# Kernel optimization log

Hardware: AMD Instinct MI355X
Metric: run time of the kernel (lower is better)

The kernel has to match this reference:

```python
import jax, jax.numpy as jnp
import numpy as np

N = 100000       # nodes
E = 1600000      # edges (before self loops)
G = 64           # graphs in batch
IN, HID, OUT = 128, 64, 16
NEG_SLOPE = 0.2  # PyG GATConv default


def setup_inputs() -> dict:
    key = jax.random.key(0)
    ks = jax.random.split(key, 16)
    s = 0.1  # weight init scale
    return {
        "x": jax.random.normal(ks[0], (N, IN), dtype=jnp.float32),
        "edge_index": jax.random.randint(ks[1], (2, E), 0, N, dtype=jnp.int32),
        "batch": jnp.sort(jax.random.randint(ks[2], (N,), 0, G, dtype=jnp.int32)),
        "W1": jax.random.normal(ks[3], (IN, 2 * HID), dtype=jnp.float32) * s,
        "a_src1": jax.random.normal(ks[4], (2, HID), dtype=jnp.float32) * s,
        "a_dst1": jax.random.normal(ks[5], (2, HID), dtype=jnp.float32) * s,
        "b1": jax.random.normal(ks[6], (2 * HID,), dtype=jnp.float32) * s,
        "W2": jax.random.normal(ks[7], (2 * HID, HID), dtype=jnp.float32) * s,
        "a_src2": jax.random.normal(ks[8], (1, HID), dtype=jnp.float32) * s,
        "a_dst2": jax.random.normal(ks[9], (1, HID), dtype=jnp.float32) * s,
        "b2": jax.random.normal(ks[10], (HID,), dtype=jnp.float32) * s,
        "dw1": jax.random.normal(ks[11], (HID, HID), dtype=jnp.float32) * s,
        "db1": jax.random.normal(ks[12], (HID,), dtype=jnp.float32) * s,
        "dw2": jax.random.normal(ks[13], (HID, OUT), dtype=jnp.float32) * s,
        "db2": jax.random.normal(ks[14], (OUT,), dtype=jnp.float32) * s,
    }


def gat_conv(x, src, dst, W, a_src, a_dst, b):
    """PyG GATConv (concat=True, self-loops already appended to src/dst)."""
    n = x.shape[0]
    heads, out = a_src.shape
    h = (x @ W).reshape(n, heads, out)                       # [N,H,O]
    e_src = jnp.einsum("nho,ho->nh", h, a_src)               # [N,H]
    e_dst = jnp.einsum("nho,ho->nh", h, a_dst)
    e = jax.nn.leaky_relu(e_src[src] + e_dst[dst], NEG_SLOPE)  # [E',H]
    # segment softmax over incoming edges of each destination node
    m = jax.lax.stop_gradient(jax.ops.segment_max(e, dst, num_segments=n))
    a = jnp.exp(e - m[dst])
    denom = jax.ops.segment_sum(a, dst, num_segments=n)
    alpha = a / denom[dst]                                   # [E',H]
    msg = h[src] * alpha[:, :, None]                         # [E',H,O]
    agg = jax.ops.segment_sum(msg, dst, num_segments=n)      # [N,H,O]
    return agg.reshape(n, heads * out) + b


def reference(x, edge_index, batch, W1, a_src1, a_dst1, b1, W2, a_src2, a_dst2,
              b2, dw1, db1, dw2, db2):
    n = x.shape[0]
    loops = jnp.arange(n, dtype=edge_index.dtype)            # add_self_loops=True
    src = jnp.concatenate([edge_index[0], loops])
    dst = jnp.concatenate([edge_index[1], loops])

    h = jax.nn.relu(gat_conv(x, src, dst, W1, a_src1, a_dst1, b1))   # [N,128]
    h = gat_conv(h, src, dst, W2, a_src2, a_dst2, b2)                # [N,64]

    # global mean pool over graphs
    cnt = jax.ops.segment_sum(jnp.ones((n,), h.dtype), batch, num_segments=G)
    pooled = jax.ops.segment_sum(h, batch, num_segments=G)
    pooled = pooled / jnp.maximum(cnt, 1.0)[:, None]                  # [G,64]

    # decoder MLP (dropout inactive in eval)
    z = jax.nn.relu(pooled @ dw1 + db1)
    return z @ dw2 + db2                                              # [G,16]
```

## Files before the change

### kernel.cpp

```cpp
#include <hip/hip_runtime.h>
#include <stdint.h>


#define LRELU(x) ((x) > 0.f ? (x) : 0.2f * (x))
#define LOG2E 1.4426950408889634f
#define BCAP 3072
#define PSLICE 8

typedef short bf8 __attribute__((ext_vector_type(8)));
typedef float f32x4 __attribute__((ext_vector_type(4)));
typedef float f32x2 __attribute__((ext_vector_type(2)));

__device__ __forceinline__ uint16_t f2bf(float f) {
  uint32_t u = __float_as_uint(f);
  u += 0x7fff + ((u >> 16) & 1);
  return (uint16_t)(u >> 16);
}
__device__ __forceinline__ uint32_t pack2bf(float a, float b) {
  return (uint32_t)f2bf(a) | ((uint32_t)f2bf(b) << 16);
}
__device__ __forceinline__ uint8_t f2fp8(float v) {
  return (uint8_t)(__builtin_amdgcn_cvt_pk_fp8_f32(v, v, 0, false) & 0xff);
}
__device__ __forceinline__ void fp8x4_to_f32(uint32_t v, float* o) {
  f32x2 lo = __builtin_amdgcn_cvt_pk_f32_fp8(v, false);
  f32x2 hi = __builtin_amdgcn_cvt_pk_f32_fp8(v, true);
  o[0] = lo[0]; o[1] = lo[1]; o[2] = hi[0]; o[3] = hi[1];
}


__global__ __launch_bounds__(256) void scatter_cvt_kernel(
    const int* __restrict__ ei, int* __restrict__ bcur,
    uint32_t* __restrict__ bpack, const float* __restrict__ W1,
    const float* __restrict__ W2, uint16_t* __restrict__ WT1,
    uint16_t* __restrict__ WT2, int E, int E2, int shift, int nb, int gCH) {
  int blk = blockIdx.x;
  int t = threadIdx.x;
  if (blk >= gCH) {
    int idx = (blk - gCH) * 256 + t;
    if (idx < 128 * 128) {
      int n = idx >> 7, k = idx & 127;
      WT1[idx] = f2bf(W1[(size_t)k * 128 + n]);
    } else if (idx < 128 * 128 + 64 * 128) {
      int j = idx - 128 * 128;
      int n = j >> 7, k = j & 127;
      WT2[j] = f2bf(W2[(size_t)k * 64 + n]);
    }
    return;
  }
  __shared__ int lh[1024];
  __shared__ int lb[1024];
  for (int i = t; i < 1024; i += 256) lh[i] = 0;
  __syncthreads();
  int base = blk * 4096;
  int bszm1 = (1 << shift) - 1;
  uint32_t pk[16];
  int rk[16], bk[16];
#pragma unroll
  for (int u = 0; u < 16; ++u) {
    int e = base + u * 256 + t;
    if (e < E2) {
      int s, d;
      if (e < E) { s = ei[e]; d = ei[E + e]; } else { s = d = e - E; }
      bk[u] = d >> shift;
      pk[u] = ((uint32_t)s << shift) | (uint32_t)(d & bszm1);
      rk[u] = atomicAdd(&lh[bk[u]], 1);
    } else rk[u] = -1;
  }
  __syncthreads();
  for (int i = t; i < nb; i += 256) {
    int c = lh[i];
    lb[i] = c ? atomicAdd(&bcur[i], c) : 0;
  }
  __syncthreads();
#pragma unroll
  for (int u = 0; u < 16; ++u) {
    if (rk[u] >= 0) {
      int pos = lb[bk[u]] + rk[u];
      if (pos < BCAP) bpack[(size_t)bk[u] * BCAP + pos] = pk[u];
    }
  }
}


__device__ __forceinline__ void bfinal_body(const uint32_t* __restrict__ bpack,
                                            const int* __restrict__ bcur,
                                            int2* __restrict__ off2,
                                            int* __restrict__ ssrc, int N,
                                            int shift, int b) {
  __shared__ int hist[512];
  __shared__ int loff[512];
  __shared__ int ssc[256];
  __shared__ int lsrc[BCAP];
  int t = threadIdx.x;
  int bsz = 1 << shift;
  int node0 = b << shift;
  int e0 = b * BCAP;
  int cnt = min(bcur[b], BCAP);
  for (int i = t; i < bsz; i += 256) hist[i] = 0;
  __syncthreads();
  uint32_t pe[12];
  int ne = 0;
#pragma unroll
  for (int j = 0; j < 12; ++j) {
    int i = j * 256 + t;
    if (i < cnt) { pe[j] = bpack[(size_t)b * BCAP + i]; ne = j + 1; }
  }
  int bszm1 = bsz - 1;
  for (int j = 0; j < ne; ++j) atomicAdd(&hist[pe[j] & bszm1], 1);
  __syncthreads();
  int per = (bsz + 255) >> 8;
  int basei = t * per;
  int va[2] = {0, 0};
  int sum = 0;
#pragma unroll 2
  for (int j = 0; j < per; ++j) {
    if (basei + j < bsz) va[j] = hist[basei + j];
    sum += va[j];
  }
  ssc[t] = sum;
  __syncthreads();
  for (int d = 1; d < 256; d <<= 1) {
    int x = (t >= d) ? ssc[t - d] : 0;
    __syncthreads();
    ssc[t] += x;
    __syncthreads();
  }
  int run = ssc[t] - sum;
#pragma unroll 2
  for (int j = 0; j < per; ++j) {
    if (basei + j < bsz) {
      loff[basei + j] = run;
      int v = node0 + basei + j;
      if (v < N) off2[v] = make_int2(e0 + run, e0 + run + va[j]);
      run += va[j];
    }
  }
  for (int i = t; i < bsz; i += 256) hist[i] = 0;
  __syncthreads();
  for (int j = 0; j < ne; ++j) {
    int ld = pe[j] & bszm1;
    int r = atomicAdd(&hist[ld], 1);
    lsrc[loff[ld] + r] = (int)(pe[j] >> shift);
  }
  __syncthreads();
  for (int i = t; i < cnt; i += 256) ssrc[e0 + i] = lsrc[i];
}


template <int N, int HEADS, int AFP32>
__device__ __forceinline__ void gemm_body(const void* __restrict__ Av,
                                          const uint16_t* __restrict__ WT,
                                          uint8_t* __restrict__ C,
                                          const float* __restrict__ aS,
                                          const float* __restrict__ aD,
                                          float* __restrict__ es,
                                          float* __restrict__ ed, int M, int blk) {
  constexpr int CT = N / 16;
  int wave = threadIdx.x >> 6;
  int lane = threadIdx.x & 63;
  int m16 = lane & 15;
  int quad = lane >> 4;
  int row_base = blk * 128 + wave * 32;
  if (row_base >= M) return;
  const uint16_t* Ab0 = (const uint16_t*)Av + (size_t)(row_base + m16) * 128;
  const uint16_t* Ab1 = Ab0 + (size_t)16 * 128;
  const float* Af0 = (const float*)Av + (size_t)(row_base + m16) * 128;
  const float* Af1 = Af0 + (size_t)16 * 128;
  f32x4 acc[2][CT] = {};
#pragma unroll
  for (int ks = 0; ks < 4; ++ks) {
    int k0 = ks * 32 + quad * 8;
    bf8 a0, a1;
    if (AFP32) {
      float4 v0 = *reinterpret_cast<const float4*>(Af0 + k0);
      float4 v1 = *reinterpret_cast<const float4*>(Af0 + k0 + 4);
      uint4 pk0;
      pk0.x = pack2bf(v0.x, v0.y); pk0.y = pack2bf(v0.z, v0.w);
      pk0.z = pack2bf(v1.x, v1.y); pk0.w = pack2bf(v1.z, v1.w);
      a0 = *reinterpret_cast<bf8*>(&pk0);
      float4 w0 = *reinterpret_cast<const float4*>(Af1 + k0);
      float4 w1 = *reinterpret_cast<const float4*>(Af1 + k0 + 4);
      uint4 pk1;
      pk1.x = pack2bf(w0.x, w0.y); pk1.y = pack2bf(w0.z, w0.w);
      pk1.z = pack2bf(w1.x, w1.y); pk1.w = pack2bf(w1.z, w1.w);
      a1 = *reinterpret_cast<bf8*>(&pk1);
    } else {
      a0 = *reinterpret_cast<const bf8*>(Ab0 + k0);
      a1 = *reinterpret_cast<const bf8*>(Ab1 + k0);
    }
#pragma unroll
    for (int c = 0; c < CT; ++c) {
      bf8 b = *reinterpret_cast<const bf8*>(WT + (size_t)(c * 16 + m16) * 128 + k0);
      acc[0][c] = __builtin_amdgcn_mfma_f32_16x16x32_bf16(a0, b, acc[0][c], 0, 0, 0);
      acc[1][c] = __builtin_amdgcn_mfma_f32_16x16x32_bf16(a1, b, acc[1][c], 0, 0, 0);
    }
  }
#pragma unroll
  for (int r = 0; r < 2; ++r) {
#pragma unroll
    for (int c = 0; c < CT; ++c) {
#pragma unroll
      for (int reg = 0; reg < 4; ++reg) {
        int row = row_base + r * 16 + quad * 4 + reg;
        C[(size_t)row * N + c * 16 + m16] = f2fp8(acc[r][c][reg]);
      }
    }
  }
  float aSv[CT], aDv[CT];
#pragma unroll
  for (int c = 0; c < CT; ++c) {
    aSv[c] = aS[c * 16 + m16];
    aDv[c] = aD[c * 16 + m16];
  }
#pragma unroll
  for (int r = 0; r < 2; ++r) {
#pragma unroll
    for (int reg = 0; reg < 4; ++reg) {
      float es0 = 0.f, es1 = 0.f, ed0 = 0.f, ed1 = 0.f;
#pragma unroll
      for (int c = 0; c < CT; ++c) {
        float v = acc[r][c][reg];
        if (HEADS == 2 && c >= CT / 2) {
          es1 = fmaf(v, aSv[c], es1);
          ed1 = fmaf(v, aDv[c], ed1);
        } else {
          es0 = fmaf(v, aSv[c], es0);
          ed0 = fmaf(v, aDv[c], ed0);
        }
      }
#pragma unroll
      for (int o = 1; o < 16; o <<= 1) {
        es0 += __shfl_xor(es0, o);
        ed0 += __shfl_xor(ed0, o);
        if (HEADS == 2) {
          es1 += __shfl_xor(es1, o);
          ed1 += __shfl_xor(ed1, o);
        }
      }
      if (m16 == 0) {
        int row = row_base + r * 16 + quad * 4 + reg;
        if (HEADS == 2) {
          es[row * 2] = es0 * LOG2E; es[row * 2 + 1] = es1 * LOG2E;
          ed[row * 2] = ed0 * LOG2E; ed[row * 2 + 1] = ed1 * LOG2E;
        } else {
          es[row] = es0 * LOG2E;
          ed[row] = ed0 * LOG2E;
        }
      }
    }
  }
}


__global__ __launch_bounds__(256) void gemm1_bfinal_kernel(
    const float* __restrict__ x, const uint16_t* __restrict__ WT1,
    uint8_t* __restrict__ hb1, const float* __restrict__ aS,
    const float* __restrict__ aD, float* __restrict__ es, float* __restrict__ ed,
    int M, const uint32_t* __restrict__ bpack, const int* __restrict__ bcur,
    int2* __restrict__ off2, int* __restrict__ ssrc, int shift, int gM) {
  int blk = blockIdx.x;
  if (blk < gM) {
    gemm_body<128, 2, 1>(x, WT1, hb1, aS, aD, es, ed, M, blk);
  } else {
    bfinal_body(bpack, bcur, off2, ssrc, M, shift, blk - gM);
  }
}

template <int N, int HEADS, int AFP32>
__global__ __launch_bounds__(256) void gemm_mfma(const void* __restrict__ Av,
                                                 const uint16_t* __restrict__ WT,
                                                 uint8_t* __restrict__ C,
                                                 const float* __restrict__ aS,
                                                 const float* __restrict__ aD,
                                                 float* __restrict__ es,
                                                 float* __restrict__ ed, int M) {
  gemm_body<N, HEADS, AFP32>(Av, WT, C, aS, aD, es, ed, M, blockIdx.x);
}


__global__ void agg1_kernel(const uint4* __restrict__ h16, const float* __restrict__ es,
                            const float2* __restrict__ ed, const int2* __restrict__ off2,
                            const int* __restrict__ ssrc, const float* __restrict__ b,
                            uint4* __restrict__ outb4, int n) {
  int w = __builtin_amdgcn_readfirstlane((blockIdx.x * 256 + threadIdx.x) >> 6);
  int lane = threadIdx.x & 63;
  if (w >= n) return;
  int sub = lane >> 3;
  int q = lane & 7;
  bool hi = q >= 4;
  float2 edw = ed[w];
  float edh = hi ? edw.y : edw.x;
  const float* esp = es + (hi ? 1 : 0);
  float acc[16] = {};
  float den = 0.f;
  int2 oo = off2[w];
  int e0 = oo.x, e1 = oo.y;
  int base = e0;
  for (; base + 16 <= e1; base += 16) {
    int s0 = ssrc[base + sub];
    int s1 = ssrc[base + 8 + sub];
    float ev0 = esp[2 * s0];
    float ev1 = esp[2 * s1];
    uint4 g0 = h16[(size_t)s0 * 8 + q];
    uint4 g1 = h16[(size_t)s1 * 8 + q];
    float a0 = exp2f(LRELU(ev0 + edh));
    float a1 = exp2f(LRELU(ev1 + edh));
    den += a0 + a1;
    float f0[16], f1[16];
    fp8x4_to_f32(g0.x, f0); fp8x4_to_f32(g0.y, f0 + 4);
    fp8x4_to_f32(g0.z, f0 + 8); fp8x4_to_f32(g0.w, f0 + 12);
    fp8x4_to_f32(g1.x, f1); fp8x4_to_f32(g1.y, f1 + 4);
    fp8x4_to_f32(g1.z, f1 + 8); fp8x4_to_f32(g1.w, f1 + 12);
#pragma unroll
    for (int j = 0; j < 16; ++j) acc[j] = fmaf(a0, f0[j], acc[j]);
#pragma unroll
    for (int j = 0; j < 16; ++j) acc[j] = fmaf(a1, f1[j], acc[j]);
  }
  if (base + 8 <= e1) {
    int s0 = ssrc[base + sub];
    float ev0 = esp[2 * s0];
    uint4 g0 = h16[(size_t)s0 * 8 + q];
    float a0 = exp2f(LRELU(ev0 + edh));
    den += a0;
    float f0[16];
    fp8x4_to_f32(g0.x, f0); fp8x4_to_f32(g0.y, f0 + 4);
    fp8x4_to_f32(g0.z, f0 + 8); fp8x4_to_f32(g0.w, f0 + 12);
#pragma unroll
    for (int j = 0; j < 16; ++j) acc[j] = fmaf(a0, f0[j], acc[j]);
    base += 8;
  }
  int e = base + sub;
  if (e < e1) {
    int s0 = ssrc[e];
    float ev0 = esp[2 * s0];
    uint4 g0 = h16[(size_t)s0 * 8 + q];
    float a0 = exp2f(LRELU(ev0 + edh));
    den += a0;
    float f0[16];
    fp8x4_to_f32(g0.x, f0); fp8x4_to_f32(g0.y, f0 + 4);
    fp8x4_to_f32(g0.z, f0 + 8); fp8x4_to_f32(g0.w, f0 + 12);
#pragma unroll
    for (int j = 0; j < 16; ++j) acc[j] = fmaf(a0, f0[j], acc[j]);
  }
#pragma unroll
  for (int m = 8; m <= 32; m <<= 1) {
    den += __shfl_xor(den, m);
#pragma unroll
    for (int j = 0; j < 16; ++j) acc[j] += __shfl_xor(acc[j], m);
  }
  if (sub == 0) {
    float inv = 1.0f / den;
    float o[16];
#pragma unroll
    for (int k = 0; k < 4; ++k) {
      float4 bb = reinterpret_cast<const float4*>(b)[q * 4 + k];
      o[k * 4 + 0] = fmaxf(fmaf(acc[k * 4 + 0], inv, bb.x), 0.f);
      o[k * 4 + 1] = fmaxf(fmaf(acc[k * 4 + 1], inv, bb.y), 0.f);
      o[k * 4 + 2] = fmaxf(fmaf(acc[k * 4 + 2], inv, bb.z), 0.f);
      o[k * 4 + 3] = fmaxf(fmaf(acc[k * 4 + 3], inv, bb.w), 0.f);
    }
    uint4 oA, oB;
    oA.x = pack2bf(o[0], o[1]);   oA.y = pack2bf(o[2], o[3]);
    oA.z = pack2bf(o[4], o[5]);   oA.w = pack2bf(o[6], o[7]);
    oB.x = pack2bf(o[8], o[9]);   oB.y = pack2bf(o[10], o[11]);
    oB.z = pack2bf(o[12], o[13]); oB.w = pack2bf(o[14], o[15]);
    outb4[(size_t)w * 16 + q * 2] = oA;
    outb4[(size_t)w * 16 + q * 2 + 1] = oB;
  }
}


__global__ void agg2_pool_kernel(const uint2* __restrict__ h8,
                                 const float* __restrict__ es,
                                 const float* __restrict__ ed,
                                 const int2* __restrict__ off2,
                                 const int* __restrict__ ssrc,
                                 const float* __restrict__ b,
                                 const int* __restrict__ batch,
                                 float* __restrict__ pooled, int gstride, int n) {
  int w = __builtin_amdgcn_readfirstlane((blockIdx.x * 256 + threadIdx.x) >> 6);
  int wave = threadIdx.x >> 6;
  int lane = threadIdx.x & 63;
  bool act = (w < n);
  int sub = lane >> 3;
  int q = lane & 7;
  __shared__ float red[4][64];
  __shared__ int gidS[4];
  float acc[8] = {};
  float den = 1.f;
  if (act) {
    float edw = ed[w];
    den = 0.f;
    int2 oo = off2[w];
    int e0 = oo.x, e1 = oo.y;
    int base = e0;
    for (; base + 16 <= e1; base += 16) {
      int s0 = ssrc[base + sub];
      int s1 = ssrc[base + 8 + sub];
      float ev0 = es[s0];
      float ev1 = es[s1];
      uint2 g0 = h8[(size_t)s0 * 8 + q];
      uint2 g1 = h8[(size_t)s1 * 8 + q];
      float a0 = exp2f(LRELU(ev0 + edw));
      float a1 = exp2f(LRELU(ev1 + edw));
      den += a0 + a1;
      float f0[8], f1[8];
      fp8x4_to_f32(g0.x, f0); fp8x4_to_f32(g0.y, f0 + 4);
      fp8x4_to_f32(g1.x, f1); fp8x4_to_f32(g1.y, f1 + 4);
#pragma unroll
      for (int j = 0; j < 8; ++j) acc[j] = fmaf(a0, f0[j], acc[j]);
#pragma unroll
      for (int j = 0; j < 8; ++j) acc[j] = fmaf(a1, f1[j], acc[j]);
    }
    if (base + 8 <= e1) {
      int s0 = ssrc[base + sub];
      float ev0 = es[s0];
      uint2 g0 = h8[(size_t)s0 * 8 + q];
      float a0 = exp2f(LRELU(ev0 + edw));
      den += a0;
      float f0[8];
      fp8x4_to_f32(g0.x, f0); fp8x4_to_f32(g0.y, f0 + 4);
#pragma unroll
      for (int j = 0; j < 8; ++j) acc[j] = fmaf(a0, f0[j], acc[j]);
      base += 8;
    }
    int e = base + sub;
    if (e < e1) {
      int s0 = ssrc[e];
      float ev0 = es[s0];
      uint2 g0 = h8[(size_t)s0 * 8 + q];
      float a0 = exp2f(LRELU(ev0 + edw));
      den += a0;
      float f0[8];
      fp8x4_to_f32(g0.x, f0); fp8x4_to_f32(g0.y, f0 + 4);
#pragma unroll
      for (int j = 0; j < 8; ++j) acc[j] = fmaf(a0, f0[j], acc[j]);
    }
#pragma unroll
    for (int m = 8; m <= 32; m <<= 1) {
      den += __shfl_xor(den, m);
#pragma unroll
      for (int j = 0; j < 8; ++j) acc[j] += __shfl_xor(acc[j], m);
    }
    if (sub == 0) {
      float inv = 1.0f / den;
      float4 b0 = reinterpret_cast<const float4*>(b)[q * 2];
      float4 b1 = reinterpret_cast<const float4*>(b)[q * 2 + 1];
      red[wave][q * 8 + 0] = fmaf(acc[0], inv, b0.x);
      red[wave][q * 8 + 1] = fmaf(acc[1], inv, b0.y);
      red[wave][q * 8 + 2] = fmaf(acc[2], inv, b0.z);
      red[wave][q * 8 + 3] = fmaf(acc[3], inv, b0.w);
      red[wave][q * 8 + 4] = fmaf(acc[4], inv, b1.x);
      red[wave][q * 8 + 5] = fmaf(acc[5], inv, b1.y);
      red[wave][q * 8 + 6] = fmaf(acc[6], inv, b1.z);
      red[wave][q * 8 + 7] = fmaf(acc[7], inv, b1.w);
    }
  }
  if (lane == 0) gidS[wave] = act ? batch[w] : -1;
  __syncthreads();
  float* pslice = pooled + (size_t)(blockIdx.x & (PSLICE - 1)) * gstride;
  int g0 = gidS[0];
  bool uni = (g0 >= 0) & (gidS[1] == g0) & (gidS[2] == g0) & (gidS[3] == g0);
  int t = threadIdx.x;
  if (uni) {
    if (t < 64) {
      float s = red[0][t] + red[1][t] + red[2][t] + red[3][t];
      atomicAdd(&pslice[g0 * 64 + t], s);
    }
  } else {
    int wv = t >> 6, c = t & 63;
    int g = gidS[wv];
    if (g >= 0) atomicAdd(&pslice[g * 64 + c], red[wv][c]);
  }
}


__device__ __forceinline__ int lowerb(const int* __restrict__ a, int n, int v) {
  int lo = 0, hi = n;
  while (lo < hi) {
    int mid = (lo + hi) >> 1;
    if (a[mid] < v) lo = mid + 1; else hi = mid;
  }
  return lo;
}

__global__ void mlp_kernel(const float* __restrict__ pooled, int gstride,
                           const int* __restrict__ batch, int n,
                           const float* __restrict__ dw1, const float* __restrict__ db1,
                           const float* __restrict__ dw2, const float* __restrict__ db2,
                           float* __restrict__ out) {
  int g = blockIdx.x;
  int c = threadIdx.x;
  __shared__ float P[64];
  __shared__ float Z[64];
  __shared__ int cntS;
  if (c == 0) cntS = lowerb(batch, n, g + 1) - lowerb(batch, n, g);
  __syncthreads();
  float inv = 1.0f / fmaxf((float)cntS, 1.0f);
  float p = 0.f;
#pragma unroll
  for (int s = 0; s < PSLICE; ++s) p += pooled[(size_t)s * gstride + g * 64 + c];
  P[c] = p * inv;
  __syncthreads();
  float s = db1[c];
#pragma unroll
  for (int k = 0; k < 64; ++k) s = fmaf(P[k], dw1[k * 64 + c], s);
  Z[c] = fmaxf(s, 0.f);
  __syncthreads();
  if (c < 16) {
    float s2 = db2[c];
#pragma unroll
    for (int k = 0; k < 64; ++k) s2 = fmaf(Z[k], dw2[k * 16 + c], s2);
    out[g * 16 + c] = s2;
  }
}


extern "C" void kernel_launch(void* const* d_in, const int* in_sizes, int n_in,
                              void* d_out, int out_size, void* d_ws, size_t ws_size,
                              hipStream_t stream) {
  const float* x      = (const float*)d_in[0];
  const int*   ei     = (const int*)d_in[1];
  const int*   batch  = (const int*)d_in[2];
  const float* W1     = (const float*)d_in[3];
  const float* a_src1 = (const float*)d_in[4];
  const float* a_dst1 = (const float*)d_in[5];
  const float* b1     = (const float*)d_in[6];
  const float* W2     = (const float*)d_in[7];
  const float* a_src2 = (const float*)d_in[8];
  const float* a_dst2 = (const float*)d_in[9];
  const float* b2     = (const float*)d_in[10];
  const float* dw1    = (const float*)d_in[11];
  const float* db1    = (const float*)d_in[12];
  const float* dw2    = (const float*)d_in[13];
  const float* db2    = (const float*)d_in[14];
  float* out = (float*)d_out;

  const int N = in_sizes[2];
  const int E = in_sizes[1] / 2;
  const int E2 = E + N;
  const int G = out_size / 16;
  const int gstride = G * 64;

  int shift = 7;
  while ((N >> shift) >= 1024) ++shift;
  const int NB = ((N - 1) >> shift) + 1;

  char* ws = (char*)d_ws;
  size_t o = 0;
  auto alloc = [&](size_t bytes) {
    void* p = ws + o;
    o = (o + bytes + 255) & ~(size_t)255;
    return p;
  };
  int*      zreg   = (int*)alloc((size_t)(1024 + PSLICE * gstride) * 4);
  int*      bcur   = zreg;
  float*    pooled = (float*)(zreg + 1024);
  int2*     off2   = (int2*)alloc((size_t)N * 8);
  uint32_t* bpack  = (uint32_t*)alloc((size_t)NB * BCAP * 4);
  int*      ssrc   = (int*)alloc((size_t)NB * BCAP * 4);
  float*    es1    = (float*)alloc((size_t)N * 2 * 4);
  float*    ed1    = (float*)alloc((size_t)N * 2 * 4);
  float*    es2    = (float*)alloc((size_t)N * 4);
  float*    ed2    = (float*)alloc((size_t)N * 4);
  uint16_t* wt1b   = (uint16_t*)alloc((size_t)128 * 128 * 2);
  uint16_t* wt2b   = (uint16_t*)alloc((size_t)64 * 128 * 2);
  uint8_t*  hb1    = (uint8_t*)alloc((size_t)N * 128);
  uint8_t*  hb2    = (uint8_t*)alloc((size_t)N * 64);
  uint32_t* out1b  = (uint32_t*)alloc((size_t)N * 64 * 4);

  hipMemsetAsync(zreg, 0, (size_t)(1024 + PSLICE * gstride) * 4, stream);

  int gM   = (N + 127) / 128;
  int gW   = (N + 3) / 4;
  int gCH  = (E2 + 4095) / 4096;
  int gCVT = (128 * 128 + 64 * 128 + 255) / 256;

  scatter_cvt_kernel<<<gCH + gCVT, 256, 0, stream>>>(ei, bcur, bpack, W1, W2,
                                                     wt1b, wt2b, E, E2, shift,
                                                     NB, gCH);
  gemm1_bfinal_kernel<<<gM + NB, 256, 0, stream>>>(x, wt1b, hb1, a_src1, a_dst1,
                                                   es1, ed1, N, bpack, bcur,
                                                   off2, ssrc, shift, gM);
  agg1_kernel<<<gW, 256, 0, stream>>>((const uint4*)hb1, es1,
                                      (const float2*)ed1, off2, ssrc, b1,
                                      (uint4*)out1b, N);
  gemm_mfma<64, 1, 0><<<gM, 256, 0, stream>>>((const void*)out1b, wt2b, hb2,
                                              a_src2, a_dst2, es2, ed2, N);
  agg2_pool_kernel<<<gW, 256, 0, stream>>>((const uint2*)hb2, es2, ed2, off2,
                                           ssrc, b2, batch, pooled, gstride, N);
  mlp_kernel<<<G, 64, 0, stream>>>(pooled, gstride, batch, N, dw1, db1, dw2,
                                   db2, out);
}
```

Before: 309.7 us.

## Map one node per 8-lane group in GAT aggregation kernels instead of per wave

Both aggregation kernels now give each node to an 8-lane subgroup, so one wave handles 8 destination nodes. Each subgroup walks the node's edges serially, unrolled by 4, which removes the cross-subgroup shuffle reduction and lane underuse on low-degree nodes. The grid shrinks by 8x to match. In the pooling kernel, wave-uniform graph ids are reduced by shuffles and then through shared memory. Mixed-graph waves fall back to per-lane atomics. The cost is a serial dependency chain per node and divergence across lanes when node degrees differ.

```diff
diff --git a/kernel.cpp b/kernel.cpp
--- a/kernel.cpp
+++ b/kernel.cpp
@@ -26,6 +26,19 @@
   f32x2 lo = __builtin_amdgcn_cvt_pk_f32_fp8(v, false);
   f32x2 hi = __builtin_amdgcn_cvt_pk_f32_fp8(v, true);
   o[0] = lo[0]; o[1] = lo[1]; o[2] = hi[0]; o[3] = hi[1];
+}
+__device__ __forceinline__ void a1_edge(const uint4& gv, float av, float* acc) {
+  float f[16];
+  fp8x4_to_f32(gv.x, f);     fp8x4_to_f32(gv.y, f + 4);
+  fp8x4_to_f32(gv.z, f + 8); fp8x4_to_f32(gv.w, f + 12);
+#pragma unroll
+  for (int j = 0; j < 16; ++j) acc[j] = fmaf(av, f[j], acc[j]);
+}
+__device__ __forceinline__ void a2_edge(const uint2& gv, float av, float* acc) {
+  float f[8];
+  fp8x4_to_f32(gv.x, f); fp8x4_to_f32(gv.y, f + 4);
+#pragma unroll
+  for (int j = 0; j < 8; ++j) acc[j] = fmaf(av, f[j], acc[j]);
 }
 
 
@@ -283,91 +296,63 @@
                             const float2* __restrict__ ed, const int2* __restrict__ off2,
                             const int* __restrict__ ssrc, const float* __restrict__ b,
                             uint4* __restrict__ outb4, int n) {
-  int w = __builtin_amdgcn_readfirstlane((blockIdx.x * 256 + threadIdx.x) >> 6);
+  int wv = __builtin_amdgcn_readfirstlane((blockIdx.x * 256 + threadIdx.x) >> 6);
   int lane = threadIdx.x & 63;
+  int grp = lane >> 3;
+  int cl = lane & 7;
+  int w = wv * 8 + grp;
   if (w >= n) return;
-  int sub = lane >> 3;
-  int q = lane & 7;
-  bool hi = q >= 4;
+  bool hi = cl >= 4;
   float2 edw = ed[w];
   float edh = hi ? edw.y : edw.x;
   const float* esp = es + (hi ? 1 : 0);
   float acc[16] = {};
   float den = 0.f;
   int2 oo = off2[w];
-  int e0 = oo.x, e1 = oo.y;
-  int base = e0;
-  for (; base + 16 <= e1; base += 16) {
-    int s0 = ssrc[base + sub];
-    int s1 = ssrc[base + 8 + sub];
-    float ev0 = esp[2 * s0];
-    float ev1 = esp[2 * s1];
-    uint4 g0 = h16[(size_t)s0 * 8 + q];
-    uint4 g1 = h16[(size_t)s1 * 8 + q];
-    float a0 = exp2f(LRELU(ev0 + edh));
-    float a1 = exp2f(LRELU(ev1 + edh));
-    den += a0 + a1;
-    float f0[16], f1[16];
-    fp8x4_to_f32(g0.x, f0); fp8x4_to_f32(g0.y, f0 + 4);
-    fp8x4_to_f32(g0.z, f0 + 8); fp8x4_to_f32(g0.w, f0 + 12);
-    fp8x4_to_f32(g1.x, f1); fp8x4_to_f32(g1.y, f1 + 4);
-    fp8x4_to_f32(g1.z, f1 + 8); fp8x4_to_f32(g1.w, f1 + 12);
-#pragma unroll
-    for (int j = 0; j < 16; ++j) acc[j] = fmaf(a0, f0[j], acc[j]);
-#pragma unroll
-    for (int j = 0; j < 16; ++j) acc[j] = fmaf(a1, f1[j], acc[j]);
-  }
-  if (base + 8 <= e1) {
-    int s0 = ssrc[base + sub];
-    float ev0 = esp[2 * s0];
-    uint4 g0 = h16[(size_t)s0 * 8 + q];
-    float a0 = exp2f(LRELU(ev0 + edh));
+  int e = oo.x, e1 = oo.y;
+  for (; e + 4 <= e1; e += 4) {
+    int s0 = ssrc[e];
+    int s1 = ssrc[e + 1];
+    int s2 = ssrc[e + 2];
+    int s3 = ssrc[e + 3];
+    uint4 g0 = h16[(size_t)s0 * 8 + cl];
+    uint4 g1 = h16[(size_t)s1 * 8 + cl];
+    uint4 g2 = h16[(size_t)s2 * 8 + cl];
+    uint4 g3 = h16[(size_t)s3 * 8 + cl];
+    float a0 = exp2f(LRELU(esp[2 * s0] + edh));
+    float a1 = exp2f(LRELU(esp[2 * s1] + edh));
+    float a2 = exp2f(LRELU(esp[2 * s2] + edh));
+    float a3 = exp2f(LRELU(esp[2 * s3] + edh));
+    den += (a0 + a1) + (a2 + a3);
+    a1_edge(g0, a0, acc);
+    a1_edge(g1, a1, acc);
+    a1_edge(g2, a2, acc);
+    a1_edge(g3, a3, acc);
+  }
+  for (; e < e1; ++e) {
+    int s0 = ssrc[e];
+    uint4 g0 = h16[(size_t)s0 * 8 + cl];
+    float a0 = exp2f(LRELU(esp[2 * s0] + edh));
     den += a0;
-    float f0[16];
-    fp8x4_to_f32(g0.x, f0); fp8x4_to_f32(g0.y, f0 + 4);
-    fp8x4_to_f32(g0.z, f0 + 8); fp8x4_to_f32(g0.w, f0 + 12);
-#pragma unroll
-    for (int j = 0; j < 16; ++j) acc[j] = fmaf(a0, f0[j], acc[j]);
-    base += 8;
-  }
-  int e = base + sub;
-  if (e < e1) {
-    int s0 = ssrc[e];
-    float ev0 = esp[2 * s0];
-    uint4 g0 = h16[(size_t)s0 * 8 + q];
-    float a0 = exp2f(LRELU(ev0 + edh));
-    den += a0;
-    float f0[16];
-    fp8x4_to_f32(g0.x, f0); fp8x4_to_f32(g0.y, f0 + 4);
-    fp8x4_to_f32(g0.z, f0 + 8); fp8x4_to_f32(g0.w, f0 + 12);
-#pragma unroll
-    for (int j = 0; j < 16; ++j) acc[j] = fmaf(a0, f0[j], acc[j]);
-  }
-#pragma unroll
-  for (int m = 8; m <= 32; m <<= 1) {
-    den += __shfl_xor(den, m);
-#pragma unroll
-    for (int j = 0; j < 16; ++j) acc[j] += __shfl_xor(acc[j], m);
-  }
-  if (sub == 0) {
-    float inv = 1.0f / den;
-    float o[16];
-#pragma unroll
-    for (int k = 0; k < 4; ++k) {
-      float4 bb = reinterpret_cast<const float4*>(b)[q * 4 + k];
-      o[k * 4 + 0] = fmaxf(fmaf(acc[k * 4 + 0], inv, bb.x), 0.f);
-      o[k * 4 + 1] = fmaxf(fmaf(acc[k * 4 + 1], inv, bb.y), 0.f);
-      o[k * 4 + 2] = fmaxf(fmaf(acc[k * 4 + 2], inv, bb.z), 0.f);
-      o[k * 4 + 3] = fmaxf(fmaf(acc[k * 4 + 3], inv, bb.w), 0.f);
-    }
-    uint4 oA, oB;
-    oA.x = pack2bf(o[0], o[1]);   oA.y = pack2bf(o[2], o[3]);
-    oA.z = pack2bf(o[4], o[5]);   oA.w = pack2bf(o[6], o[7]);
-    oB.x = pack2bf(o[8], o[9]);   oB.y = pack2bf(o[10], o[11]);
-    oB.z = pack2bf(o[12], o[13]); oB.w = pack2bf(o[14], o[15]);
-    outb4[(size_t)w * 16 + q * 2] = oA;
-    outb4[(size_t)w * 16 + q * 2 + 1] = oB;
-  }
+    a1_edge(g0, a0, acc);
+  }
+  float inv = 1.0f / den;
+  float o[16];
+#pragma unroll
+  for (int k = 0; k < 4; ++k) {
+    float4 bb = reinterpret_cast<const float4*>(b)[cl * 4 + k];
+    o[k * 4 + 0] = fmaxf(fmaf(acc[k * 4 + 0], inv, bb.x), 0.f);
+    o[k * 4 + 1] = fmaxf(fmaf(acc[k * 4 + 1], inv, bb.y), 0.f);
+    o[k * 4 + 2] = fmaxf(fmaf(acc[k * 4 + 2], inv, bb.z), 0.f);
+    o[k * 4 + 3] = fmaxf(fmaf(acc[k * 4 + 3], inv, bb.w), 0.f);
+  }
+  uint4 oA, oB;
+  oA.x = pack2bf(o[0], o[1]);   oA.y = pack2bf(o[2], o[3]);
+  oA.z = pack2bf(o[4], o[5]);   oA.w = pack2bf(o[6], o[7]);
+  oB.x = pack2bf(o[8], o[9]);   oB.y = pack2bf(o[10], o[11]);
+  oB.z = pack2bf(o[12], o[13]); oB.w = pack2bf(o[14], o[15]);
+  outb4[(size_t)w * 16 + cl * 2] = oA;
+  outb4[(size_t)w * 16 + cl * 2 + 1] = oB;
 }
 
 
@@ -379,99 +364,95 @@
                                  const float* __restrict__ b,
                                  const int* __restrict__ batch,
                                  float* __restrict__ pooled, int gstride, int n) {
-  int w = __builtin_amdgcn_readfirstlane((blockIdx.x * 256 + threadIdx.x) >> 6);
-  int wave = threadIdx.x >> 6;
-  int lane = threadIdx.x & 63;
+  int t = threadIdx.x;
+  int wv = __builtin_amdgcn_readfirstlane((blockIdx.x * 256 + t) >> 6);
+  int wave = t >> 6;
+  int lane = t & 63;
+  int grp = lane >> 3;
+  int cl = lane & 7;
+  int w = wv * 8 + grp;
   bool act = (w < n);
-  int sub = lane >> 3;
-  int q = lane & 7;
   __shared__ float red[4][64];
-  __shared__ int gidS[4];
+  __shared__ int uniS[4];
+  float* pslice = pooled + (size_t)(blockIdx.x & (PSLICE - 1)) * gstride;
   float acc[8] = {};
-  float den = 1.f;
+  int g = -1;
   if (act) {
+    g = batch[w];
     float edw = ed[w];
-    den = 0.f;
+    float den = 0.f;
     int2 oo = off2[w];
-    int e0 = oo.x, e1 = oo.y;
-    int base = e0;
-    for (; base + 16 <= e1; base += 16) {
-      int s0 = ssrc[base + sub];
-      int s1 = ssrc[base + 8 + sub];
-      float ev0 = es[s0];
-      float ev1 = es[s1];
-      uint2 g0 = h8[(size_t)s0 * 8 + q];
-      uint2 g1 = h8[(size_t)s1 * 8 + q];
-      float a0 = exp2f(LRELU(ev0 + edw));
-      float a1 = exp2f(LRELU(ev1 + edw));
-      den += a0 + a1;
-      float f0[8], f1[8];
-      fp8x4_to_f32(g0.x, f0); fp8x4_to_f32(g0.y, f0 + 4);
-      fp8x4_to_f32(g1.x, f1); fp8x4_to_f32(g1.y, f1 + 4);
-#pragma unroll
-      for (int j = 0; j < 8; ++j) acc[j] = fmaf(a0, f0[j], acc[j]);
-#pragma unroll
-      for (int j = 0; j < 8; ++j) acc[j] = fmaf(a1, f1[j], acc[j]);
-    }
-    if (base + 8 <= e1) {
-      int s0 = ssrc[base + sub];
-      float ev0 = es[s0];
-      uint2 g0 = h8[(size_t)s0 * 8 + q];
-      float a0 = exp2f(LRELU(ev0 + edw));
+    int e = oo.x, e1 = oo.y;
+    for (; e + 4 <= e1; e += 4) {
+      int s0 = ssrc[e];
+      int s1 = ssrc[e + 1];
+      int s2 = ssrc[e + 2];
+      int s3 = ssrc[e + 3];
+      uint2 g0 = h8[(size_t)s0 * 8 + cl];
+      uint2 g1 = h8[(size_t)s1 * 8 + cl];
+      uint2 g2 = h8[(size_t)s2 * 8 + cl];
+      uint2 g3 = h8[(size_t)s3 * 8 + cl];
+      float a0 = exp2f(LRELU(es[s0] + edw));
+      float a1 = exp2f(LRELU(es[s1] + edw));
+      float a2 = exp2f(LRELU(es[s2] + edw));
+      float a3 = exp2f(LRELU(es[s3] + edw));
+      den += (a0 + a1) + (a2 + a3);
+      a2_edge(g0, a0, acc);
+      a2_edge(g1, a1, acc);
+      a2_edge(g2, a2, acc);
+      a2_edge(g3, a3, acc);
+    }
+    for (; e < e1; ++e) {
+      int s0 = ssrc[e];
+      uint2 g0 = h8[(size_t)s0 * 8 + cl];
+      float a0 = exp2f(LRELU(es[s0] + edw));
       den += a0;
-      float f0[8];
-      fp8x4_to_f32(g0.x, f0); fp8x4_to_f32(g0.y, f0 + 4);
-#pragma unroll
-      for (int j = 0; j < 8; ++j) acc[j] = fmaf(a0, f0[j], acc[j]);
-      base += 8;
-    }
-    int e = base + sub;
-    if (e < e1) {
-      int s0 = ssrc[e];
-      float ev0 = es[s0];
-      uint2 g0 = h8[(size_t)s0 * 8 + q];
-      float a0 = exp2f(LRELU(ev0 + edw));
-      den += a0;
-      float f0[8];
-      fp8x4_to_f32(g0.x, f0); fp8x4_to_f32(g0.y, f0 + 4);
-#pragma unroll
-      for (int j = 0; j < 8; ++j) acc[j] = fmaf(a0, f0[j], acc[j]);
-    }
+      a2_edge(g0, a0, acc);
+    }
+    float inv = 1.0f / den;
+    float4 b0 = reinterpret_cast<const float4*>(b)[cl * 2];
+    float4 b1 = reinterpret_cast<const float4*>(b)[cl * 2 + 1];
+    acc[0] = fmaf(acc[0], inv, b0.x);
+    acc[1] = fmaf(acc[1], inv, b0.y);
+    acc[2] = fmaf(acc[2], inv, b0.z);
+    acc[3] = fmaf(acc[3], inv, b0.w);
+    acc[4] = fmaf(acc[4], inv, b1.x);
+    acc[5] = fmaf(acc[5], inv, b1.y);
+    acc[6] = fmaf(acc[6], inv, b1.z);
+    acc[7] = fmaf(acc[7], inv, b1.w);
+  }
+  int g0lane = __shfl(g, 0);
+  bool same = __all(g == g0lane);
+  if (same && g0lane >= 0) {
 #pragma unroll
     for (int m = 8; m <= 32; m <<= 1) {
-      den += __shfl_xor(den, m);
 #pragma unroll
       for (int j = 0; j < 8; ++j) acc[j] += __shfl_xor(acc[j], m);
     }
-    if (sub == 0) {
-      float inv = 1.0f / den;
-      float4 b0 = reinterpret_cast<const float4*>(b)[q * 2];
-      float4 b1 = reinterpret_cast<const float4*>(b)[q * 2 + 1];
-      red[wave][q * 8 + 0] = fmaf(acc[0], inv, b0.x);
-      red[wave][q * 8 + 1] = fmaf(acc[1], inv, b0.y);
-      red[wave][q * 8 + 2] = fmaf(acc[2], inv, b0.z);
-      red[wave][q * 8 + 3] = fmaf(acc[3], inv, b0.w);
-      red[wave][q * 8 + 4] = fmaf(acc[4], inv, b1.x);
-      red[wave][q * 8 + 5] = fmaf(acc[5], inv, b1.y);
-      red[wave][q * 8 + 6] = fmaf(acc[6], inv, b1.z);
-      red[wave][q * 8 + 7] = fmaf(acc[7], inv, b1.w);
-    }
-  }
-  if (lane == 0) gidS[wave] = act ? batch[w] : -1;
-  __syncthreads();
-  float* pslice = pooled + (size_t)(blockIdx.x & (PSLICE - 1)) * gstride;
-  int g0 = gidS[0];
-  bool uni = (g0 >= 0) & (gidS[1] == g0) & (gidS[2] == g0) & (gidS[3] == g0);
-  int t = threadIdx.x;
-  if (uni) {
+    if (grp == 0) {
+#pragma unroll
+      for (int j = 0; j < 8; ++j) red[wave][cl * 8 + j] = acc[j];
+    }
+    if (lane == 0) uniS[wave] = g0lane;
+  } else {
+    if (lane == 0) uniS[wave] = same ? -1 : -2;
+    if (act && !same) {
+#pragma unroll
+      for (int j = 0; j < 8; ++j)
+        atomicAdd(&pslice[(size_t)g * 64 + cl * 8 + j], acc[j]);
+    }
+  }
+  __syncthreads();
+  int u0 = uniS[0];
+  bool allsame = (u0 >= 0) & (uniS[1] == u0) & (uniS[2] == u0) & (uniS[3] == u0);
+  if (allsame) {
     if (t < 64) {
       float s = red[0][t] + red[1][t] + red[2][t] + red[3][t];
-      atomicAdd(&pslice[g0 * 64 + t], s);
+      atomicAdd(&pslice[(size_t)u0 * 64 + t], s);
     }
   } else {
-    int wv = t >> 6, c = t & 63;
-    int g = gidS[wv];
-    if (g >= 0) atomicAdd(&pslice[g * 64 + c], red[wv][c]);
+    int gw = uniS[wave];
+    if (gw >= 0) atomicAdd(&pslice[(size_t)gw * 64 + lane], red[wave][lane]);
   }
 }
 
@@ -573,7 +554,7 @@
   hipMemsetAsync(zreg, 0, (size_t)(1024 + PSLICE * gstride) * 4, stream);
 
   int gM   = (N + 127) / 128;
-  int gW   = (N + 3) / 4;
+  int gW   = (N + 31) / 32;
   int gCH  = (E2 + 4095) / 4096;
   int gCVT = (128 * 128 + 64 * 128 + 255) / 256;
 
```

After: 264.5 us (median of 2 runs). -14.6%, faster.
